# Optimization experiments

Hardware: AMD Instinct MI355X
Metric: run time of the kernel (lower is better)

The kernel has to match this reference:

```python
import jax, jax.numpy as jnp
import numpy as np

N = 100000      # nodes
E = 1600000     # edges (avg degree 16)
D_IN = 64
D_OUT = 64
EPS = 1e-9


def setup_inputs() -> dict:
    key = jax.random.key(0)
    ks = jax.random.split(key, 12)
    x = jax.random.normal(ks[0], (N, D_IN), dtype=jnp.float32)
    edge_row = jax.random.randint(ks[1], (E,), 0, N, dtype=jnp.int32)
    edge_col = jax.random.randint(ks[2], (E,), 0, N, dtype=jnp.int32)
    # positive normalized adjacency values (~1/degree scale)
    edge_val = jax.random.uniform(ks[3], (E,), dtype=jnp.float32) / 16.0
    lim = float(np.sqrt(6.0 / (D_IN + D_OUT)))  # xavier_uniform
    W0 = jax.random.uniform(ks[4], (D_OUT, D_IN), jnp.float32, -lim, lim)
    W1 = jax.random.uniform(ks[5], (D_OUT, D_IN), jnp.float32, -lim, lim)
    b0 = jnp.zeros((D_OUT,), jnp.float32)
    b1 = jnp.zeros((D_OUT,), jnp.float32)
    scale0 = jnp.ones((D_OUT,), jnp.float32)
    scale1 = jnp.ones((D_OUT,), jnp.float32)
    offset0 = jnp.zeros((D_OUT,), jnp.float32)
    offset1 = jnp.zeros((D_OUT,), jnp.float32)
    return {"x": x, "edge_val": edge_val, "W0": W0, "b0": b0,
            "scale0": scale0, "offset0": offset0, "W1": W1, "b1": b1,
            "scale1": scale1, "offset1": offset1,
            "edge_row": edge_row, "edge_col": edge_col}


def _hop_transform(feat, W, b, scale, offset):
    # Linear (no bias in nn.Linear) + separate bias + ReLU
    h = jax.nn.relu(feat @ W.T + b)                      # [N, D_OUT]
    # custom per-row normalization ('norm' branch)
    mean = jnp.mean(h, axis=1, keepdims=True)
    var = jnp.var(h, axis=1, keepdims=True) + EPS        # unbiased=False
    return (h - mean) * scale * jax.lax.rsqrt(var) + offset


def reference(x, edge_val, W0, b0, scale0, offset0, W1, b1, scale1, offset1,
              edge_row, edge_col):
    # SpMM: out[r] = sum_{e: row[e]==r} val[e] * x[col[e]]
    msgs = edge_val[:, None] * x[edge_col]               # [E, D_IN]
    agg = jax.ops.segment_sum(msgs, edge_row, num_segments=N)
    # order=1: hop-0 uses raw features, hop-1 uses aggregated features
    h0 = _hop_transform(x, W0, b0, scale0, offset0)
    h1 = _hop_transform(agg, W1, b1, scale1, offset1)
    # aggr='mean' -> elementwise sum of partial features
    return h0 + h1
```

## Files before the change

### kernel.cpp

```cpp
#include <hip/hip_runtime.h>

#define NN 100000
#define NE 1600000
#define DD 64
#define NB   391
#define NBK1 391
#define BCAP 4608
#define SCAP 6656
#define GCAP 2400000
#define NK3  1563

__device__ __forceinline__ unsigned short f2bfu(float f) {
    union { float f; unsigned u; } c; c.f = f;
    unsigned lsb = (c.u >> 16) & 1u;
    c.u += 0x7FFFu + lsb;
    return (unsigned short)(c.u >> 16);
}

typedef short v8s __attribute__((ext_vector_type(8)));
typedef float v4f __attribute__((ext_vector_type(4)));

__global__ __launch_bounds__(256) void init_kernel(
    const float* __restrict__ W0, const float* __restrict__ W1,
    int* __restrict__ gbcur, int* __restrict__ gtail,
    unsigned short* __restrict__ wb0, unsigned short* __restrict__ wb1)
{
    int i = blockIdx.x * 256 + threadIdx.x;
    if (i < NB) gbcur[i] = 0;
    if (i == 0) *gtail = 0;
    if (i < DD * DD) { wb0[i] = f2bfu(W0[i]); wb1[i] = f2bfu(W1[i]); }
}

__global__ __launch_bounds__(512) void bucket_scatter_kernel(
    const int* __restrict__ row, const int* __restrict__ col,
    const float* __restrict__ val, int* __restrict__ gbcur,
    int2* __restrict__ bslab)
{
    __shared__ int hist[NB];
    int b = blockIdx.x, t = threadIdx.x;
    if (t < NB) hist[t] = 0;
    __syncthreads();

    int4 r[2], c[2]; float4 v[2]; bool ok[2];
#pragma unroll
    for (int h = 0; h < 2; ++h) {
        int e = b * 4096 + h * 2048 + t * 4;
        ok[h] = (e + 3 < NE);
        if (ok[h]) {
            r[h] = *(const int4*)(row + e);
            c[h] = *(const int4*)(col + e);
            v[h] = *(const float4*)(val + e);
            atomicAdd(&hist[r[h].x >> 8], 1);
            atomicAdd(&hist[r[h].y >> 8], 1);
            atomicAdd(&hist[r[h].z >> 8], 1);
            atomicAdd(&hist[r[h].w >> 8], 1);
        }
    }
    __syncthreads();
    if (t < NB) {
        int cnt = hist[t];
        hist[t] = cnt ? atomicAdd(&gbcur[t], cnt) : 0;
    }
    __syncthreads();
#pragma unroll
    for (int h = 0; h < 2; ++h) {
        if (ok[h]) {
            int b0_ = r[h].x >> 8, b1_ = r[h].y >> 8;
            int b2_ = r[h].z >> 8, b3_ = r[h].w >> 8;
            int q0 = atomicAdd(&hist[b0_], 1);
            int q1 = atomicAdd(&hist[b1_], 1);
            int q2 = atomicAdd(&hist[b2_], 1);
            int q3 = atomicAdd(&hist[b3_], 1);
            if (q0 < BCAP) bslab[(size_t)b0_ * BCAP + q0] =
                make_int2(c[h].x | ((r[h].x & 255) << 17), __float_as_int(v[h].x));
            if (q1 < BCAP) bslab[(size_t)b1_ * BCAP + q1] =
                make_int2(c[h].y | ((r[h].y & 255) << 17), __float_as_int(v[h].y));
            if (q2 < BCAP) bslab[(size_t)b2_ * BCAP + q2] =
                make_int2(c[h].z | ((r[h].z & 255) << 17), __float_as_int(v[h].z));
            if (q3 < BCAP) bslab[(size_t)b3_ * BCAP + q3] =
                make_int2(c[h].w | ((r[h].w & 255) << 17), __float_as_int(v[h].w));
        }
    }
}

__global__ __launch_bounds__(512) void row_sort_kernel(
    const int* __restrict__ gbcur, const int2* __restrict__ bslab,
    int* __restrict__ gtail, int2* __restrict__ gsorted,
    int* __restrict__ meta)
{
    __shared__ int2 sorted[SCAP];
    __shared__ int cnt[256];
    __shared__ int pscan[256];
    __shared__ int rcur[256];
    __shared__ int pstart[257];
    __shared__ int sh_base8;

    int b = blockIdx.x, t = threadIdx.x;
    int nb = min(gbcur[b], BCAP);
    const int2* bp = bslab + (size_t)b * BCAP;

    int2 rec[9]; int rl[9]; int nr = 0;
    if (t < 256) cnt[t] = 0;
    __syncthreads();
#pragma unroll
    for (int k = 0; k < 9; ++k) {
        int i = t + k * 512;
        if (i < nb) {
            rec[nr] = bp[i];
            rl[nr] = (rec[nr].x >> 17) & 255;
            atomicAdd(&cnt[rl[nr]], 1);
            ++nr;
        }
    }
    __syncthreads();
    if (t < 256) pscan[t] = (cnt[t] + 7) & ~7;
    __syncthreads();
    for (int off = 1; off < 256; off <<= 1) {
        int u = 0;
        if (t < 256 && t >= off) u = pscan[t - off];
        __syncthreads();
        if (t < 256) pscan[t] += u;
        __syncthreads();
    }
    if (t < 256) pstart[t + 1] = pscan[t];
    if (t == 0) {
        pstart[0] = 0;
        sh_base8 = atomicAdd(gtail, pscan[255] >> 3);
    }
    __syncthreads();
    int base8 = sh_base8;
    if (t < 256) {
        rcur[t] = pstart[t];
        int s = pstart[t] + cnt[t], e = pstart[t + 1];
        for (int j = s; j < e; ++j) sorted[j] = make_int2(0, 0);
        int n = b * 256 + t;
        int cc = min((e - pstart[t]) >> 3, 16);
        int s8 = base8 + (pstart[t] >> 3);
        meta[n] = (s8 << 5) | cc;
    }
    __syncthreads();
#pragma unroll
    for (int k = 0; k < 9; ++k) {
        if (k < nr) {
            int pos = atomicAdd(&rcur[rl[k]], 1);
            if (pos < SCAP) sorted[pos] = make_int2(rec[k].x & 0x1FFFF, rec[k].y);
        }
    }
    __syncthreads();
    int tp = pscan[255];
    int gb = base8 * 8;
    for (int i = t; i < tp; i += 512) {
        int gi = gb + i;
        if (gi < GCAP) gsorted[gi] = sorted[i];
    }
}

__global__ __launch_bounds__(256, 8) void pull_mfma_kernel(
    const float* __restrict__ x, const int* __restrict__ meta,
    const int2* __restrict__ gsorted,
    const unsigned short* __restrict__ wb0, const unsigned short* __restrict__ wb1,
    const float* __restrict__ b0, const float* __restrict__ s0, const float* __restrict__ o0,
    const float* __restrict__ b1, const float* __restrict__ s1, const float* __restrict__ o1,
    float* __restrict__ out)
{
    __shared__ int2 ebuf[4][128];
    __shared__ unsigned aggt[4][16][36];

    int t = threadIdx.x, lane = t & 63, wv = t >> 6;
    int sub = lane & 15, q = lane >> 4;
    int nb0 = blockIdx.x * 64 + wv * 16;
    if (nb0 >= NN) return;

    for (int rr = 0; rr < 16; ++rr) {
        int mt = meta[nb0 + rr];
        int cc = mt & 31;
        const int2* rp = gsorted + ((size_t)(mt >> 5) << 3);
        int plen = cc * 8;
        if (lane < plen) ebuf[wv][lane] = rp[lane];
        if (64 + lane < plen) ebuf[wv][64 + lane] = rp[64 + lane];

        float4 acc = make_float4(0.f, 0.f, 0.f, 0.f);
        int ch = 0;
        for (; ch + 2 <= cc; ch += 2) {
            int2 r0 = ebuf[wv][ch * 8 + q];
            int2 r1 = ebuf[wv][ch * 8 + 4 + q];
            int2 r2 = ebuf[wv][ch * 8 + 8 + q];
            int2 r3 = ebuf[wv][ch * 8 + 12 + q];
            float4 f0 = *(const float4*)(x + (size_t)r0.x * DD + sub * 4);
            float4 f1 = *(const float4*)(x + (size_t)r1.x * DD + sub * 4);
            float4 f2 = *(const float4*)(x + (size_t)r2.x * DD + sub * 4);
            float4 f3 = *(const float4*)(x + (size_t)r3.x * DD + sub * 4);
            float v0 = __int_as_float(r0.y), v1 = __int_as_float(r1.y);
            float v2 = __int_as_float(r2.y), v3 = __int_as_float(r3.y);
            acc.x = fmaf(v0, f0.x, acc.x); acc.y = fmaf(v0, f0.y, acc.y);
            acc.z = fmaf(v0, f0.z, acc.z); acc.w = fmaf(v0, f0.w, acc.w);
            acc.x = fmaf(v1, f1.x, acc.x); acc.y = fmaf(v1, f1.y, acc.y);
            acc.z = fmaf(v1, f1.z, acc.z); acc.w = fmaf(v1, f1.w, acc.w);
            acc.x = fmaf(v2, f2.x, acc.x); acc.y = fmaf(v2, f2.y, acc.y);
            acc.z = fmaf(v2, f2.z, acc.z); acc.w = fmaf(v2, f2.w, acc.w);
            acc.x = fmaf(v3, f3.x, acc.x); acc.y = fmaf(v3, f3.y, acc.y);
            acc.z = fmaf(v3, f3.z, acc.z); acc.w = fmaf(v3, f3.w, acc.w);
        }
        if (ch < cc) {
            int2 r0 = ebuf[wv][ch * 8 + q];
            int2 r1 = ebuf[wv][ch * 8 + 4 + q];
            float4 f0 = *(const float4*)(x + (size_t)r0.x * DD + sub * 4);
            float4 f1 = *(const float4*)(x + (size_t)r1.x * DD + sub * 4);
            float v0 = __int_as_float(r0.y), v1 = __int_as_float(r1.y);
            acc.x = fmaf(v0, f0.x, acc.x); acc.y = fmaf(v0, f0.y, acc.y);
            acc.z = fmaf(v0, f0.z, acc.z); acc.w = fmaf(v0, f0.w, acc.w);
            acc.x = fmaf(v1, f1.x, acc.x); acc.y = fmaf(v1, f1.y, acc.y);
            acc.z = fmaf(v1, f1.z, acc.z); acc.w = fmaf(v1, f1.w, acc.w);
        }
        acc.x += __shfl_xor(acc.x, 16, 64); acc.y += __shfl_xor(acc.y, 16, 64);
        acc.z += __shfl_xor(acc.z, 16, 64); acc.w += __shfl_xor(acc.w, 16, 64);
        acc.x += __shfl_xor(acc.x, 32, 64); acc.y += __shfl_xor(acc.y, 32, 64);
        acc.z += __shfl_xor(acc.z, 32, 64); acc.w += __shfl_xor(acc.w, 32, 64);
        if (q == 0) {
            uint2 pk;
            pk.x = (unsigned)f2bfu(acc.x) | ((unsigned)f2bfu(acc.y) << 16);
            pk.y = (unsigned)f2bfu(acc.z) | ((unsigned)f2bfu(acc.w) << 16);
            *(uint2*)&aggt[wv][rr][sub * 2] = pk;
        }
    }

    v8s ax[2], aa[2];
#pragma unroll
    for (int ks = 0; ks < 2; ++ks) {
        const float* px = x + (size_t)(nb0 + sub) * DD + ks * 32 + q * 8;
        float4 a0 = *(const float4*)px, a1 = *(const float4*)(px + 4);
        v8s w;
        w[0] = (short)f2bfu(a0.x); w[1] = (short)f2bfu(a0.y);
        w[2] = (short)f2bfu(a0.z); w[3] = (short)f2bfu(a0.w);
        w[4] = (short)f2bfu(a1.x); w[5] = (short)f2bfu(a1.y);
        w[6] = (short)f2bfu(a1.z); w[7] = (short)f2bfu(a1.w);
        ax[ks] = w;
        aa[ks] = *(const v8s*)&aggt[wv][sub][ks * 16 + q * 4];
    }

    float h0v[4][4], h1v[4][4];
    float sr0[4] = {0,0,0,0}, sq0[4] = {0,0,0,0};
    float sr1[4] = {0,0,0,0}, sq1[4] = {0,0,0,0};
#pragma unroll
    for (int dt = 0; dt < 4; ++dt) {
        int nidx = dt * 16 + sub;
        float bi0 = b0[nidx], bi1 = b1[nidx];
        v8s w00 = *(const v8s*)(wb0 + nidx * 64 + q * 8);
        v8s w01 = *(const v8s*)(wb0 + nidx * 64 + 32 + q * 8);
        v8s w10 = *(const v8s*)(wb1 + nidx * 64 + q * 8);
        v8s w11 = *(const v8s*)(wb1 + nidx * 64 + 32 + q * 8);
        v4f c0 = (v4f){bi0, bi0, bi0, bi0};
        v4f c1 = (v4f){bi1, bi1, bi1, bi1};
        c0 = __builtin_amdgcn_mfma_f32_16x16x32_bf16(ax[0], w00, c0, 0, 0, 0);
        c0 = __builtin_amdgcn_mfma_f32_16x16x32_bf16(ax[1], w01, c0, 0, 0, 0);
        c1 = __builtin_amdgcn_mfma_f32_16x16x32_bf16(aa[0], w10, c1, 0, 0, 0);
        c1 = __builtin_amdgcn_mfma_f32_16x16x32_bf16(aa[1], w11, c1, 0, 0, 0);
#pragma unroll
        for (int r = 0; r < 4; ++r) {
            float h = fmaxf(c0[r], 0.f); h0v[dt][r] = h; sr0[r] += h; sq0[r] += h * h;
            float g = fmaxf(c1[r], 0.f); h1v[dt][r] = g; sr1[r] += g; sq1[r] += g * g;
        }
    }
#pragma unroll
    for (int off = 1; off < 16; off <<= 1) {
#pragma unroll
        for (int r = 0; r < 4; ++r) {
            sr0[r] += __shfl_xor(sr0[r], off, 64);
            sq0[r] += __shfl_xor(sq0[r], off, 64);
            sr1[r] += __shfl_xor(sr1[r], off, 64);
            sq1[r] += __shfl_xor(sq1[r], off, 64);
        }
    }

    float scl0[4], scl1[4], ofs0[4], ofs1[4];
#pragma unroll
    for (int dt = 0; dt < 4; ++dt) {
        int nidx = dt * 16 + sub;
        scl0[dt] = s0[nidx]; scl1[dt] = s1[nidx];
        ofs0[dt] = o0[nidx]; ofs1[dt] = o1[nidx];
    }

    const float inv = 1.0f / 64.0f;
#pragma unroll
    for (int r = 0; r < 4; ++r) {
        float m0 = sr0[r] * inv;
        float v0 = fmaxf(sq0[r] * inv - m0 * m0, 0.f) + 1e-9f;
        float m1 = sr1[r] * inv;
        float v1 = fmaxf(sq1[r] * inv - m1 * m1, 0.f) + 1e-9f;
        float rs0 = rsqrtf(v0), rs1 = rsqrtf(v1);
        int node = nb0 + q * 4 + r;
#pragma unroll
        for (int dt = 0; dt < 4; ++dt) {
            float rv = (h0v[dt][r] - m0) * scl0[dt] * rs0 + ofs0[dt]
                     + (h1v[dt][r] - m1) * scl1[dt] * rs1 + ofs1[dt];
            out[(size_t)node * DD + dt * 16 + sub] = rv;
        }
    }
}

extern "C" void kernel_launch(void* const* d_in, const int* in_sizes, int n_in,
                              void* d_out, int out_size, void* d_ws, size_t ws_size,
                              hipStream_t stream) {
    const float* x  = (const float*)d_in[0];
    const float* ev = (const float*)d_in[1];
    const float* W0 = (const float*)d_in[2];
    const float* b0 = (const float*)d_in[3];
    const float* s0 = (const float*)d_in[4];
    const float* o0 = (const float*)d_in[5];
    const float* W1 = (const float*)d_in[6];
    const float* b1 = (const float*)d_in[7];
    const float* s1 = (const float*)d_in[8];
    const float* o1 = (const float*)d_in[9];
    const int* row = (const int*)d_in[10];
    const int* col = (const int*)d_in[11];

    char* wsb = (char*)d_ws;
    int*  gbcur = (int*)wsb;
    int*  gtail = (int*)(wsb + 1600);
    unsigned short* wb0 = (unsigned short*)(wsb + 1664);
    unsigned short* wb1 = (unsigned short*)(wsb + 9856);
    int*  meta  = (int*)(wsb + 18176);
    int2* bslab = (int2*)(wsb + 418816);
    int2* gsorted = (int2*)(wsb + 14832640);

    init_kernel<<<16, 256, 0, stream>>>(W0, W1, gbcur, gtail, wb0, wb1);
    bucket_scatter_kernel<<<NBK1, 512, 0, stream>>>(row, col, ev, gbcur, bslab);
    row_sort_kernel<<<NB, 512, 0, stream>>>(gbcur, bslab, gtail, gsorted, meta);
    pull_mfma_kernel<<<NK3, 256, 0, stream>>>(
        x, meta, gsorted, wb0, wb1, b0, s0, o0, b1, s1, o1, (float*)d_out);
}
```

Measured before the change: 213.1 us.

## Pre-convert x to bf16 for gathers and stage bucket scatter through LDS

Adds a kernel that converts x to bf16 once, so the SpMM gather loads half the bytes per neighbour row and the hop-0 MFMA operand is read directly without per-element conversion. The bucket scatter now sorts each block's 4096 edges by bucket in shared memory (prefix scan plus local cursors) before writing them out, making the global slab writes contiguous per bucket instead of scattered. The extra conversion pass and added scan/sync cost are traded against lower gather bandwidth, and aggregation now uses bf16-rounded neighbour features.

Result: faster. 193.3 us (-9.3%).

```diff
diff --git a/kernel.cpp b/kernel.cpp
--- a/kernel.cpp
+++ b/kernel.cpp
@@ -4,7 +4,6 @@
 #define NE 1600000
 #define DD 64
 #define NB   391
-#define NBK1 391
 #define BCAP 4608
 #define SCAP 6656
 #define GCAP 2400000
@@ -31,55 +30,94 @@
     if (i < DD * DD) { wb0[i] = f2bfu(W0[i]); wb1[i] = f2bfu(W1[i]); }
 }
 
-__global__ __launch_bounds__(512) void bucket_scatter_kernel(
+__global__ __launch_bounds__(256) void x2bf_kernel(
+    const float* __restrict__ x, unsigned short* __restrict__ xb)
+{
+    int i = (blockIdx.x * 256 + threadIdx.x) * 8;
+    float4 a = *(const float4*)(x + i);
+    float4 b = *(const float4*)(x + i + 4);
+    uint4 o;
+    o.x = (unsigned)f2bfu(a.x) | ((unsigned)f2bfu(a.y) << 16);
+    o.y = (unsigned)f2bfu(a.z) | ((unsigned)f2bfu(a.w) << 16);
+    o.z = (unsigned)f2bfu(b.x) | ((unsigned)f2bfu(b.y) << 16);
+    o.w = (unsigned)f2bfu(b.z) | ((unsigned)f2bfu(b.w) << 16);
+    *(uint4*)(xb + i) = o;
+}
+
+__global__ __launch_bounds__(512) void bin_scatter_kernel(
     const int* __restrict__ row, const int* __restrict__ col,
     const float* __restrict__ val, int* __restrict__ gbcur,
     int2* __restrict__ bslab)
 {
-    __shared__ int hist[NB];
+    __shared__ int2 rbuf[4096];
+    __shared__ unsigned short bkts[4096];
+    __shared__ int pscan[512];
+    __shared__ int cnt[NB];
+    __shared__ int pst[NB];
+    __shared__ int cur[NB];
+    __shared__ int gbase[NB];
+
     int b = blockIdx.x, t = threadIdx.x;
-    if (t < NB) hist[t] = 0;
+    int e0 = b * 4096;
+
+    for (int i = t; i < NB; i += 512) cnt[i] = 0;
     __syncthreads();
 
     int4 r[2], c[2]; float4 v[2]; bool ok[2];
 #pragma unroll
     for (int h = 0; h < 2; ++h) {
-        int e = b * 4096 + h * 2048 + t * 4;
+        int e = e0 + t * 8 + h * 4;
         ok[h] = (e + 3 < NE);
         if (ok[h]) {
             r[h] = *(const int4*)(row + e);
             c[h] = *(const int4*)(col + e);
             v[h] = *(const float4*)(val + e);
-            atomicAdd(&hist[r[h].x >> 8], 1);
-            atomicAdd(&hist[r[h].y >> 8], 1);
-            atomicAdd(&hist[r[h].z >> 8], 1);
-            atomicAdd(&hist[r[h].w >> 8], 1);
-        }
-    }
-    __syncthreads();
+            atomicAdd(&cnt[r[h].x >> 8], 1);
+            atomicAdd(&cnt[r[h].y >> 8], 1);
+            atomicAdd(&cnt[r[h].z >> 8], 1);
+            atomicAdd(&cnt[r[h].w >> 8], 1);
+        }
+    }
+    __syncthreads();
+    pscan[t] = (t < NB) ? cnt[t] : 0;
+    __syncthreads();
+    for (int off = 1; off < 512; off <<= 1) {
+        int u = (t >= off) ? pscan[t - off] : 0;
+        __syncthreads();
+        pscan[t] += u;
+        __syncthreads();
+    }
     if (t < NB) {
-        int cnt = hist[t];
-        hist[t] = cnt ? atomicAdd(&gbcur[t], cnt) : 0;
+        int st = pscan[t] - cnt[t];
+        pst[t] = st;
+        cur[t] = st;
+        gbase[t] = cnt[t] ? atomicAdd(&gbcur[t], cnt[t]) : 0;
     }
     __syncthreads();
 #pragma unroll
     for (int h = 0; h < 2; ++h) {
         if (ok[h]) {
-            int b0_ = r[h].x >> 8, b1_ = r[h].y >> 8;
-            int b2_ = r[h].z >> 8, b3_ = r[h].w >> 8;
-            int q0 = atomicAdd(&hist[b0_], 1);
-            int q1 = atomicAdd(&hist[b1_], 1);
-            int q2 = atomicAdd(&hist[b2_], 1);
-            int q3 = atomicAdd(&hist[b3_], 1);
-            if (q0 < BCAP) bslab[(size_t)b0_ * BCAP + q0] =
-                make_int2(c[h].x | ((r[h].x & 255) << 17), __float_as_int(v[h].x));
-            if (q1 < BCAP) bslab[(size_t)b1_ * BCAP + q1] =
-                make_int2(c[h].y | ((r[h].y & 255) << 17), __float_as_int(v[h].y));
-            if (q2 < BCAP) bslab[(size_t)b2_ * BCAP + q2] =
-                make_int2(c[h].z | ((r[h].z & 255) << 17), __float_as_int(v[h].z));
-            if (q3 < BCAP) bslab[(size_t)b3_ * BCAP + q3] =
-                make_int2(c[h].w | ((r[h].w & 255) << 17), __float_as_int(v[h].w));
-        }
+            int bk, pos;
+            bk = r[h].x >> 8; pos = atomicAdd(&cur[bk], 1);
+            rbuf[pos] = make_int2(c[h].x | ((r[h].x & 255) << 17), __float_as_int(v[h].x));
+            bkts[pos] = (unsigned short)bk;
+            bk = r[h].y >> 8; pos = atomicAdd(&cur[bk], 1);
+            rbuf[pos] = make_int2(c[h].y | ((r[h].y & 255) << 17), __float_as_int(v[h].y));
+            bkts[pos] = (unsigned short)bk;
+            bk = r[h].z >> 8; pos = atomicAdd(&cur[bk], 1);
+            rbuf[pos] = make_int2(c[h].z | ((r[h].z & 255) << 17), __float_as_int(v[h].z));
+            bkts[pos] = (unsigned short)bk;
+            bk = r[h].w >> 8; pos = atomicAdd(&cur[bk], 1);
+            rbuf[pos] = make_int2(c[h].w | ((r[h].w & 255) << 17), __float_as_int(v[h].w));
+            bkts[pos] = (unsigned short)bk;
+        }
+    }
+    __syncthreads();
+    int ntot = pscan[511];
+    for (int i = t; i < ntot; i += 512) {
+        int bk = bkts[i];
+        int gi = gbase[bk] + (i - pst[bk]);
+        if (gi < BCAP) bslab[(size_t)bk * BCAP + gi] = rbuf[i];
     }
 }
 
@@ -155,8 +193,14 @@
     }
 }
 
+#define BF4FMA(G, VV, ACC) { \
+    ACC.x = fmaf(VV, __uint_as_float((G).x << 16), ACC.x); \
+    ACC.y = fmaf(VV, __uint_as_float((G).x & 0xFFFF0000u), ACC.y); \
+    ACC.z = fmaf(VV, __uint_as_float((G).y << 16), ACC.z); \
+    ACC.w = fmaf(VV, __uint_as_float((G).y & 0xFFFF0000u), ACC.w); }
+
 __global__ __launch_bounds__(256, 8) void pull_mfma_kernel(
-    const float* __restrict__ x, const int* __restrict__ meta,
+    const unsigned short* __restrict__ xb, const int* __restrict__ meta,
     const int2* __restrict__ gsorted,
     const unsigned short* __restrict__ wb0, const unsigned short* __restrict__ wb1,
     const float* __restrict__ b0, const float* __restrict__ s0, const float* __restrict__ o0,
@@ -186,31 +230,22 @@
             int2 r1 = ebuf[wv][ch * 8 + 4 + q];
             int2 r2 = ebuf[wv][ch * 8 + 8 + q];
             int2 r3 = ebuf[wv][ch * 8 + 12 + q];
-            float4 f0 = *(const float4*)(x + (size_t)r0.x * DD + sub * 4);
-            float4 f1 = *(const float4*)(x + (size_t)r1.x * DD + sub * 4);
-            float4 f2 = *(const float4*)(x + (size_t)r2.x * DD + sub * 4);
-            float4 f3 = *(const float4*)(x + (size_t)r3.x * DD + sub * 4);
+            uint2 g0 = *(const uint2*)(xb + (size_t)r0.x * DD + sub * 4);
+            uint2 g1 = *(const uint2*)(xb + (size_t)r1.x * DD + sub * 4);
+            uint2 g2 = *(const uint2*)(xb + (size_t)r2.x * DD + sub * 4);
+            uint2 g3 = *(const uint2*)(xb + (size_t)r3.x * DD + sub * 4);
             float v0 = __int_as_float(r0.y), v1 = __int_as_float(r1.y);
             float v2 = __int_as_float(r2.y), v3 = __int_as_float(r3.y);
-            acc.x = fmaf(v0, f0.x, acc.x); acc.y = fmaf(v0, f0.y, acc.y);
-            acc.z = fmaf(v0, f0.z, acc.z); acc.w = fmaf(v0, f0.w, acc.w);
-            acc.x = fmaf(v1, f1.x, acc.x); acc.y = fmaf(v1, f1.y, acc.y);
-            acc.z = fmaf(v1, f1.z, acc.z); acc.w = fmaf(v1, f1.w, acc.w);
-            acc.x = fmaf(v2, f2.x, acc.x); acc.y = fmaf(v2, f2.y, acc.y);
-            acc.z = fmaf(v2, f2.z, acc.z); acc.w = fmaf(v2, f2.w, acc.w);
-            acc.x = fmaf(v3, f3.x, acc.x); acc.y = fmaf(v3, f3.y, acc.y);
-            acc.z = fmaf(v3, f3.z, acc.z); acc.w = fmaf(v3, f3.w, acc.w);
+            BF4FMA(g0, v0, acc); BF4FMA(g1, v1, acc);
+            BF4FMA(g2, v2, acc); BF4FMA(g3, v3, acc);
         }
         if (ch < cc) {
             int2 r0 = ebuf[wv][ch * 8 + q];
             int2 r1 = ebuf[wv][ch * 8 + 4 + q];
-            float4 f0 = *(const float4*)(x + (size_t)r0.x * DD + sub * 4);
-            float4 f1 = *(const float4*)(x + (size_t)r1.x * DD + sub * 4);
+            uint2 g0 = *(const uint2*)(xb + (size_t)r0.x * DD + sub * 4);
+            uint2 g1 = *(const uint2*)(xb + (size_t)r1.x * DD + sub * 4);
             float v0 = __int_as_float(r0.y), v1 = __int_as_float(r1.y);
-            acc.x = fmaf(v0, f0.x, acc.x); acc.y = fmaf(v0, f0.y, acc.y);
-            acc.z = fmaf(v0, f0.z, acc.z); acc.w = fmaf(v0, f0.w, acc.w);
-            acc.x = fmaf(v1, f1.x, acc.x); acc.y = fmaf(v1, f1.y, acc.y);
-            acc.z = fmaf(v1, f1.z, acc.z); acc.w = fmaf(v1, f1.w, acc.w);
+            BF4FMA(g0, v0, acc); BF4FMA(g1, v1, acc);
         }
         acc.x += __shfl_xor(acc.x, 16, 64); acc.y += __shfl_xor(acc.y, 16, 64);
         acc.z += __shfl_xor(acc.z, 16, 64); acc.w += __shfl_xor(acc.w, 16, 64);
@@ -227,14 +262,7 @@
     v8s ax[2], aa[2];
 #pragma unroll
     for (int ks = 0; ks < 2; ++ks) {
-        const float* px = x + (size_t)(nb0 + sub) * DD + ks * 32 + q * 8;
-        float4 a0 = *(const float4*)px, a1 = *(const float4*)(px + 4);
-        v8s w;
-        w[0] = (short)f2bfu(a0.x); w[1] = (short)f2bfu(a0.y);
-        w[2] = (short)f2bfu(a0.z); w[3] = (short)f2bfu(a0.w);
-        w[4] = (short)f2bfu(a1.x); w[5] = (short)f2bfu(a1.y);
-        w[6] = (short)f2bfu(a1.z); w[7] = (short)f2bfu(a1.w);
-        ax[ks] = w;
+        ax[ks] = *(const v8s*)(xb + (size_t)(nb0 + sub) * DD + ks * 32 + q * 8);
         aa[ks] = *(const v8s*)&aggt[wv][sub][ks * 16 + q * 4];
     }
 
@@ -320,12 +348,14 @@
     unsigned short* wb0 = (unsigned short*)(wsb + 1664);
     unsigned short* wb1 = (unsigned short*)(wsb + 9856);
     int*  meta  = (int*)(wsb + 18176);
-    int2* bslab = (int2*)(wsb + 418816);
-    int2* gsorted = (int2*)(wsb + 14832640);
+    unsigned short* xb = (unsigned short*)(wsb + 418816);
+    int2* bslab = (int2*)(wsb + 13218816);
+    int2* gsorted = (int2*)(wsb + 27632640);
 
     init_kernel<<<16, 256, 0, stream>>>(W0, W1, gbcur, gtail, wb0, wb1);
-    bucket_scatter_kernel<<<NBK1, 512, 0, stream>>>(row, col, ev, gbcur, bslab);
+    x2bf_kernel<<<3125, 256, 0, stream>>>(x, xb);
+    bin_scatter_kernel<<<NB, 512, 0, stream>>>(row, col, ev, gbcur, bslab);
     row_sort_kernel<<<NB, 512, 0, stream>>>(gbcur, bslab, gtail, gsorted, meta);
     pull_mfma_kernel<<<NK3, 256, 0, stream>>>(
-        x, meta, gsorted, wb0, wb1, b0, s0, o0, b1, s1, o1, (float*)d_out);
-}
+        xb, meta, gsorted, wb0, wb1, b0, s0, o0, b1, s1, o1, (float*)d_out);
+}
```
